# Optimization experiments

Measured on AMD Instinct MI355X. Metric: run time of the kernel, lower is better.

The kernel has to match this reference:

```python
import jax, jax.numpy as jnp
import numpy as np

B, L, D = 4, 2048, 1024
H, DH = 16, 64
W = 128            # window_len
CS, R = 32, 1      # chunk_size, chunk_rank
CACHE = 2048
NCC = CACHE // CS * R   # compressed cache vectors (64)
NCB = L // CS * R       # compressed block vectors (64)
NC = NCC + NCB          # total compressed vectors (128)
NQ = L // CS            # query chunks (64)
T = L // W              # query tiles (16)
NEG = jnp.float32(-1e30)


def _ln(x, g, b, eps=1e-5):
    m = x.mean(-1, keepdims=True)
    v = ((x - m) ** 2).mean(-1, keepdims=True)
    return (x - m) * jax.lax.rsqrt(v + eps) * g + b


def _scores(x, Wd, bd):
    # dconv_1 + per-chunk softmax over chunk_size positions
    b = x.shape[0]; nc = x.shape[1] // CS
    s = (x @ Wd + bd).reshape(b, nc, CS, H, R)
    s = jnp.transpose(s, (0, 3, 1, 4, 2))          # b,H,nc,R,CS
    return jax.nn.softmax(s.astype(jnp.float32), axis=-1).astype(x.dtype)


def _compress(x, sc):
    b = x.shape[0]; nc = x.shape[1] // CS
    xv = jnp.transpose(x.reshape(b, nc, CS, H, DH), (0, 3, 1, 2, 4))  # b,H,nc,CS,DH
    return (sc @ xv).reshape(b, H, nc * R, DH)


def _heads(x):
    b, l, _ = x.shape
    return jnp.transpose(x.reshape(b, l, H, DH), (0, 2, 1, 3))


def _rel_shift(x):
    # Transformer-XL style relative shift, chunk variant (zeros enter from padding)
    b = x.shape[0]; nc = x.shape[-1]
    x5 = jnp.transpose(x.reshape(b, H, NQ, CS, nc), (0, 1, 3, 2, 4))  # b,H,CS,NQ,nc
    xp = jnp.pad(x5, ((0, 0), (0, 0), (0, 0), (0, 0), (0, R))).reshape(b, H, CS, NQ * (nc + R))
    idx = NQ * R + jnp.arange(NQ)[:, None] * nc + jnp.arange(nc)[None, :]
    out = jnp.take(xp, idx.reshape(-1), axis=-1).reshape(b, H, CS, NQ, nc)
    return jnp.transpose(out, (0, 1, 3, 2, 4)).reshape(b, H, L, nc)


def _forward(h, h_cache, key_pe, pos_win, Wq, Wk, Wv, Wo, Wd, bd, Wr, br, Wrc, brc,
             r_r_bias, r_w_bias, g_dproj, b_dproj, g_win, b_win, mask):
    b = h.shape[0]
    q = _heads(h @ Wq) / np.float32(np.sqrt(DH))       # b,H,L,DH (pre-scaled)

    # --- compressed cache keys/values ---
    hcc = _compress(h_cache, _scores(h_cache, Wd, bd))           # b,H,NCC,DH
    hcm = jnp.transpose(hcc, (0, 2, 1, 3)).reshape(b, -1, D)
    k_cache = _heads(_ln(hcm @ Wk, g_dproj, b_dproj))
    v_cache = _heads(_ln(hcm @ Wv, g_dproj, b_dproj))

    # --- sliding window keys/values (last W of cache + current block) ---
    k_bp = h @ Wk
    v_bp = h @ Wv
    hw = h_cache[:, -W:]
    k_win = _ln(jnp.concatenate([hw @ Wk, k_bp], 1), g_win, b_win)   # b, W+L, D
    v_win = _ln(jnp.concatenate([hw @ Wv, v_bp], 1), g_win, b_win)

    # --- compressed current-block keys/values ---
    sc = _scores(h, Wd, bd)
    k_bpc = _heads(_ln(jnp.transpose(_compress(k_bp, sc), (0, 2, 1, 3)).reshape(b, -1, D), g_dproj, b_dproj))
    v_bpc = _heads(_ln(jnp.transpose(_compress(v_bp, sc), (0, 2, 1, 3)).reshape(b, -1, D), g_dproj, b_dproj))
    k_comp = jnp.concatenate([k_cache, k_bpc], 2)     # b,H,NC,DH
    v_comp = jnp.concatenate([v_cache, v_bpc], 2)

    # --- windowed attention (tiled, as_strided equivalent via gather) ---
    ti = jnp.arange(T)[:, None] * W + jnp.arange(2 * W)[None, :]     # (T, 2W)
    k_t = jnp.transpose(k_win[:, ti].reshape(b, T, 2 * W, H, DH), (0, 3, 1, 2, 4))  # b,H,T,2W,DH
    v_t = jnp.transpose(v_win[:, ti].reshape(b, T, 2 * W, H, DH), (0, 3, 1, 2, 4))
    q_t = q.reshape(b, H, T, W, DH)
    aw = jnp.einsum('bhtqd,bhtkd->bhtqk', q_t + r_w_bias, k_t)       # b,H,T,W,2W
    # diagonal extraction: row q keeps cols q+1 .. q+W (the W causal window keys)
    dcol = jnp.arange(W)[:, None] + 1 + jnp.arange(W)[None, :]       # (W, W)
    aw = jnp.take_along_axis(aw, dcol[None, None, None], axis=-1).reshape(b, H, L, W)
    pos_t = (pos_win @ Wr + br).reshape(W, H, DH)
    aw = aw + jnp.einsum('bhld,whd->bhlw', q + r_r_bias, pos_t)

    # --- compressed (chunk) attention ---
    ac = jnp.einsum('bhld,bhcd->bhlc', q, k_comp)
    pos_c = (key_pe @ Wrc + brc).reshape(NC, H, DH)
    ac = ac + _rel_shift(jnp.einsum('bhld,chd->bhlc', q, pos_c))
    ac = jnp.where(mask, NEG, ac.reshape(b, H, NQ, CS, NC)).reshape(b, H, L, NC)

    # --- joint softmax over [compressed | window] ---
    full = jax.nn.softmax(jnp.concatenate([ac, aw], -1).astype(jnp.float32), -1).astype(h.dtype)
    ac, aw = full[..., :NC], full[..., NC:]

    # --- put_tiles: scatter window probs back to tiled 2W layout (inverse of diag extract) ---
    awt = aw.reshape(b, H, T, W, W)
    awp = jnp.pad(awt, ((0, 0), (0, 0), (0, 0), (0, 0), (1, W)))     # last dim 1+2W, zeros outside band
    col = jnp.clip(jnp.arange(2 * W)[None, :] - jnp.arange(W)[:, None], 0, 2 * W)
    aw_t = jnp.take_along_axis(awp, col[None, None, None], axis=-1)  # b,H,T,W,2W

    out = jnp.einsum('bhlc,bhcd->bhld', ac, v_comp) + \
          jnp.einsum('bhtqk,bhtkd->bhtqd', aw_t, v_t).reshape(b, H, L, DH)
    out = jnp.transpose(out, (0, 2, 1, 3)).reshape(b, L, D)
    return out @ Wo


def setup_inputs() -> dict:
    key = jax.random.key(0)
    ks = jax.random.split(key, 16)
    p = lambda i, shape: jax.random.normal(ks[i], shape, jnp.float32) * 0.02
    inp = dict(
        h=jax.random.normal(ks[0], (B, L, D), jnp.float32),
        h_cache=jax.random.normal(ks[1], (B, CACHE, D), jnp.float32),
        key_pe=jax.random.normal(ks[2], (NC, D), jnp.float32),
        pos_embed_window=jax.random.normal(ks[3], (W, D), jnp.float32),
        Wq=p(4, (D, D)), Wk=p(5, (D, D)), Wv=p(6, (D, D)), Wo=p(7, (D, D)),
        Wd=p(8, (D, H * R)), bd=jnp.zeros((H * R,), jnp.float32),
        Wr=p(9, (D, D)), br=jnp.zeros((D,), jnp.float32),
        Wrc=p(10, (D, D)), brc=jnp.zeros((D,), jnp.float32),
        r_r_bias=p(11, (1, H, 1, DH)), r_w_bias=p(12, (1, H, 1, 1, DH)),
        g_dproj=jnp.ones((D,), jnp.float32), b_dproj=jnp.zeros((D,), jnp.float32),
        g_win=jnp.ones((D,), jnp.float32), b_win=jnp.zeros((D,), jnp.float32),
    )
    # causal mask over compressed vectors: bp chunk c visible to query chunk j only if c < j
    jq = jnp.arange(NQ)[:, None]
    cc = jnp.arange(NCB // R)[None, :]
    mbp = jnp.repeat(cc >= jq, R, axis=1)                         # (NQ, NCB)
    mask = jnp.concatenate([jnp.zeros((NQ, NCC), bool), mbp], axis=1)
    inp['chunked_attn_mask'] = mask[None, None, :, None, :]       # (1,1,NQ,1,NC)
    return inp


def reference(h, h_cache, key_pe, pos_embed_window, Wq, Wk, Wv, Wo, Wd, bd, Wr, br,
              Wrc, brc, r_r_bias, r_w_bias, g_dproj, b_dproj, g_win, b_win,
              chunked_attn_mask):
    return _forward(h, h_cache, key_pe, pos_embed_window, Wq, Wk, Wv, Wo, Wd, bd,
                    Wr, br, Wrc, brc, r_r_bias, r_w_bias, g_dproj, b_dproj,
                    g_win, b_win, chunked_attn_mask)
```

## Files before the change

kernel.cpp:

```cpp
#include <hip/hip_runtime.h>


typedef unsigned short u16;
typedef __attribute__((ext_vector_type(8))) short short8;
typedef __attribute__((ext_vector_type(4))) float f32x4;

#define NEGINF -1e30f

__device__ __forceinline__ float bf2f(u16 u) {
    union { unsigned int i; float f; } v; v.i = ((unsigned int)u) << 16; return v.f;
}
__device__ __forceinline__ u16 f2bf(float f) {
    union { float fl; unsigned int i; } v; v.fl = f;
    unsigned int x = v.i;
    return (u16)((x + 0x7fffu + ((x >> 16) & 1u)) >> 16);
}
__device__ __forceinline__ short8 ldg8(const u16* p) { return *(const short8*)p; }

__device__ __forceinline__ void async16(const u16* g, u16* l) {
    __builtin_amdgcn_global_load_lds(
        (const __attribute__((address_space(1))) unsigned int*)g,
        (__attribute__((address_space(3))) unsigned int*)l, 16, 0, 0);
}

__global__ __launch_bounds__(256) void cast_fuse(
    const float* __restrict__ h, const float* __restrict__ hc,
    const float* __restrict__ pos_w, const float* __restrict__ key_pe,
    const float* __restrict__ Wd,
    u16* __restrict__ hB, u16* __restrict__ hcwB,
    u16* __restrict__ pwB, u16* __restrict__ kpeB, u16* __restrict__ WdB,
    const float* __restrict__ W0, const float* __restrict__ W1,
    const float* __restrict__ W2, const float* __restrict__ W3,
    const float* __restrict__ W4, const float* __restrict__ W5,
    u16* __restrict__ D0, u16* __restrict__ D1, u16* __restrict__ D2,
    u16* __restrict__ D3, u16* __restrict__ D4, u16* __restrict__ D5)
{
    const int bx = blockIdx.x, tid = threadIdx.x;
    __shared__ float t[32][33];

    if (bx < 8192) {
        int i = bx * 256 + tid;
        float4 v = ((const float4*)h)[i];
        u16* o = hB + (long)i * 4;
        o[0] = f2bf(v.x); o[1] = f2bf(v.y); o[2] = f2bf(v.z); o[3] = f2bf(v.w);
    } else if (bx < 8704) {
        int i = (bx - 8192) * 256 + tid;
        int flat = i * 4;
        int b = flat >> 17, r = (flat >> 10) & 127, c = flat & 1023;
        float4 v = *(const float4*)(hc + ((long)b * 2048 + 1920 + r) * 1024 + c);
        u16* o = hcwB + (long)flat;
        o[0] = f2bf(v.x); o[1] = f2bf(v.y); o[2] = f2bf(v.z); o[3] = f2bf(v.w);
    } else if (bx < 8832) {
        int i = (bx - 8704) * 256 + tid;
        float4 v = ((const float4*)pos_w)[i];
        u16* o = pwB + (long)i * 4;
        o[0] = f2bf(v.x); o[1] = f2bf(v.y); o[2] = f2bf(v.z); o[3] = f2bf(v.w);
    } else if (bx < 8960) {
        int i = (bx - 8832) * 256 + tid;
        float4 v = ((const float4*)key_pe)[i];
        u16* o = kpeB + (long)i * 4;
        o[0] = f2bf(v.x); o[1] = f2bf(v.y); o[2] = f2bf(v.z); o[3] = f2bf(v.w);
    } else if (bx < 9024) {
        int e = (bx - 8960) * 256 + tid;
        if (e < 16384) WdB[(e & 15) * 1024 + (e >> 4)] = f2bf(Wd[e]);
    } else {
        const int t6 = bx - 9024;
        const int z = t6 >> 10;
        const int rem = t6 & 1023;
        const int bxx = rem & 31, byy = rem >> 5;
        const float* W = (z == 0) ? W0 : (z == 1) ? W1 : (z == 2) ? W2
                       : (z == 3) ? W3 : (z == 4) ? W4 : W5;
        u16* WT = (z == 0) ? D0 : (z == 1) ? D1 : (z == 2) ? D2
                : (z == 3) ? D3 : (z == 4) ? D4 : D5;
        const int tx = tid & 31, ty = tid >> 5;
        #pragma unroll
        for (int p = 0; p < 4; ++p) {
            int k = byy * 32 + ty + p * 8;
            t[ty + p * 8][tx] = W[(long)k * 1024 + bxx * 32 + tx];
        }
        __syncthreads();
        #pragma unroll
        for (int p = 0; p < 4; ++p) {
            int n = ty + p * 8;
            WT[((long)(bxx * 32 + n)) * 1024 + byy * 32 + tx] = f2bf(t[tx][n]);
        }
    }
}

__global__ __launch_bounds__(512) void gemm_qkv_big(
    const u16* __restrict__ A, const u16* __restrict__ Bt,
    u16* __restrict__ q_ws, u16* __restrict__ kbp, u16* __restrict__ vbp)
{
    const int tid = threadIdx.x;
    const int bm = blockIdx.x, bn = blockIdx.y;
    const int K = 1024, NT = 32;

    __shared__ __align__(16) u16 smem[65536 / 2];
    u16* const As = smem;
    u16* const Bs = smem + 16384;

    const int lane = tid & 63, wv = tid >> 6;
    const int l15 = lane & 15, quad = lane >> 4;
    const int wm = (wv >> 2) * 128, wn = (wv & 3) * 64;

    f32x4 acc[8][4];
    #pragma unroll
    for (int i = 0; i < 8; ++i)
        #pragma unroll
        for (int j = 0; j < 4; ++j) acc[i][j] = (f32x4){0.f, 0.f, 0.f, 0.f};

    const int r_in = lane >> 2;
    const int col8 = (((lane & 3) ^ ((lane >> 3) & 3)) * 8);
    const bool isA = (wv < 4);
    const int crow0 = (isA ? wv : wv - 4) * 64;
    const u16* gb = isA ? (A + (long)(bm * 256 + crow0 + r_in) * K)
                        : (Bt + (long)(bn * 256 + crow0 + r_in) * K);
    const u16* s0 = gb + col8;
    const u16* s1 = s0 + (long)16 * K;
    const u16* s2 = s0 + (long)32 * K;
    const u16* s3 = s0 + (long)48 * K;
    u16* const lb = (isA ? As : Bs) + crow0 * 32;

    auto stage = [&](int buf) {
        u16* d = lb + buf * 8192;
        async16(s0, d);
        async16(s1, d + 512);
        async16(s2, d + 1024);
        async16(s3, d + 1536);
        s0 += 32; s1 += 32; s2 += 32; s3 += 32;
    };

    const int ssl = (quad ^ ((l15 >> 1) & 3)) * 8;

    stage(0);
    for (int t = 0; t < NT; ++t) {
        __builtin_amdgcn_s_barrier();
        if (t + 1 < NT) {
            stage((t + 1) & 1);
            asm volatile("s_waitcnt vmcnt(4) lgkmcnt(0)\ns_barrier" ::: "memory");
        } else {
            asm volatile("s_waitcnt vmcnt(0) lgkmcnt(0)\ns_barrier" ::: "memory");
        }
        const u16* as = As + (t & 1) * 8192;
        const u16* bs = Bs + (t & 1) * 8192;
        short8 af[8], bfr[4];
        #pragma unroll
        for (int i = 0; i < 8; ++i)
            af[i] = *(const short8*)&as[(wm + i * 16 + l15) * 32 + ssl];
        #pragma unroll
        for (int j = 0; j < 4; ++j)
            bfr[j] = *(const short8*)&bs[(wn + j * 16 + l15) * 32 + ssl];
        #pragma unroll
// ... 62 lines not shown
        async16(a_src  + k0, &As[cur * 4096 + lofs0]);                          \
        async16(a_src2 + k0, &As[cur * 4096 + lofs1]);                          \
        async16(b_src  + k0, &Bs[cur * 4096 + lofs0]);                          \
        async16(b_src2 + k0, &Bs[cur * 4096 + lofs1]);                          \
    };                                                                          \
    stage(0, 0); stage(1, 1);                                                   \
    const int ssl = (quad ^ ((l15 >> 1) & 3)) * 8;                              \
    int cur = 0;                                                                \
    for (int t = 0; t < NT; ++t) {                                              \
        if (t == NT - 1)                                                        \
            asm volatile("s_waitcnt vmcnt(0) lgkmcnt(0)\ns_barrier" ::: "memory"); \
        else                                                                    \
            asm volatile("s_waitcnt vmcnt(4) lgkmcnt(0)\ns_barrier" ::: "memory"); \
        int nxt = cur + 2; if (nxt >= 3) nxt -= 3;                              \
        if (t + 2 < NT) stage(t + 2, nxt);                                      \
        const u16* as = &As[cur * 4096];                                        \
        const u16* bs = &Bs[cur * 4096];                                        \
        short8 af[4], bfr[4];                                                   \
        _Pragma("unroll")                                                       \
        for (int i = 0; i < 4; ++i)                                             \
            af[i] = *(const short8*)&as[(wm + i * 16 + l15) * 32 + ssl];        \
        _Pragma("unroll")                                                       \
        for (int j = 0; j < 4; ++j)                                             \
            bfr[j] = *(const short8*)&bs[(wn + j * 16 + l15) * 32 + ssl];       \
        _Pragma("unroll")                                                       \
        for (int i = 0; i < 4; ++i)                                             \
            _Pragma("unroll")                                                   \
            for (int j = 0; j < 4; ++j)                                         \
                acc[i][j] = __builtin_amdgcn_mfma_f32_16x16x32_bf16(af[i], bfr[j], acc[i][j], 0, 0, 0); \
        cur = (cur + 1 == 3) ? 0 : cur + 1;                                     \
    }                                                                           \
    EPILOGUE

__global__ __launch_bounds__(256) void gemm_out3(
    const u16* __restrict__ A, const u16* __restrict__ Bt,
    float* __restrict__ Cf)
{
    GEMM_P3_BODY({
        _Pragma("unroll")
        for (int i = 0; i < 4; ++i) {
            _Pragma("unroll")
            for (int j = 0; j < 4; ++j) {
                int col = bn * 128 + wn + j * 16 + l15;
                _Pragma("unroll")
                for (int r = 0; r < 4; ++r) {
                    int row = bm * 128 + wm + i * 16 + quad * 4 + r;
                    Cf[(long)row * 1024 + col] = acc[i][j][r];
                }
            }
        }
    })
}

struct GJob {
    const u16* A; long ab;
    const u16* Bt;
    float* Cf; u16* Cb; long cb;
    const float* bias; float scale;
    int bmN;
};

__device__ __forceinline__ void gemm_core128(
    const GJob& j, int bz, int bm, int bn, int N, int K)
{
    const int tid = threadIdx.x;
    const u16* A = j.A + (long)bz * j.ab;
    const long coff = (long)bz * j.cb;

    __shared__ __align__(16) u16 As[128 * 32];
    __shared__ __align__(16) u16 Bs[128 * 32];

    const int lane = tid & 63, wv = tid >> 6;
    const int l15 = lane & 15, quad = lane >> 4;
    const int wm = (wv & 1) * 64, wn = (wv >> 1) * 64;

    f32x4 acc[4][4];
    #pragma unroll
    for (int i = 0; i < 4; ++i)
        #pragma unroll
        for (int jx = 0; jx < 4; ++jx) acc[i][jx] = (f32x4){0.f, 0.f, 0.f, 0.f};

    const int srow = wv * 32 + (lane >> 2);
    const int scol = (lane & 3) * 8;
    const u16* a_src  = A    + (long)(bm * 128 + srow) * K + scol;
    const u16* a_src2 = a_src + (long)16 * K;
    const u16* b_src  = j.Bt + (long)(bn * 128 + srow) * K + scol;
    const u16* b_src2 = b_src + (long)16 * K;
    u16* lA0 = &As[(wv * 32) * 32];
    u16* lA1 = &As[(wv * 32 + 16) * 32];
    u16* lB0 = &Bs[(wv * 32) * 32];
    u16* lB1 = &Bs[(wv * 32 + 16) * 32];

    for (int k0 = 0; k0 < K; k0 += 32) {
        async16(a_src, lA0); async16(a_src2, lA1);
        async16(b_src, lB0); async16(b_src2, lB1);
        a_src += 32; a_src2 += 32; b_src += 32; b_src2 += 32;
        __syncthreads();
        short8 af[4], bfr[4];
        #pragma unroll
        for (int i = 0; i < 4; ++i)
            af[i] = *(const short8*)&As[(wm + i * 16 + l15) * 32 + quad * 8];
        #pragma unroll
        for (int jx = 0; jx < 4; ++jx)
            bfr[jx] = *(const short8*)&Bs[(wn + jx * 16 + l15) * 32 + quad * 8];
        #pragma unroll
        for (int i = 0; i < 4; ++i)
            #pragma unroll
            for (int jx = 0; jx < 4; ++jx)
                acc[i][jx] = __builtin_amdgcn_mfma_f32_16x16x32_bf16(af[i], bfr[jx], acc[i][jx], 0, 0, 0);
        __syncthreads();
    }

    #pragma unroll
    for (int i = 0; i < 4; ++i) {
        #pragma unroll
        for (int jx = 0; jx < 4; ++jx) {
            int col = bn * 128 + wn + jx * 16 + l15;
            float bsv = j.bias ? j.bias[col] : 0.f;
            #pragma unroll
            for (int r = 0; r < 4; ++r) {
                int row = bm * 128 + wm + i * 16 + quad * 4 + r;
                float v = acc[i][jx][r] * j.scale + bsv;
                long idx = coff + (long)row * N + col;
                if (j.Cf) j.Cf[idx] = v;
                if (j.Cb) j.Cb[idx] = f2bf(v);
            }
        }
    }
}

__global__ __launch_bounds__(256) void gemm_multi6(
    GJob j0, GJob j1, GJob j2, GJob j3, GJob j4, GJob j5,
    int n0, int n1, int n2, int n3, int n4, int N, int K)
{
    const int z = blockIdx.z;
    GJob j; int bz;
    if (z < n0)                          { j = j0; bz = z; }
    else if (z < n0 + n1)                { j = j1; bz = z - n0; }
    else if (z < n0 + n1 + n2)           { j = j2; bz = z - n0 - n1; }
    else if (z < n0 + n1 + n2 + n3)      { j = j3; bz = z - n0 - n1 - n2; }
    else if (z < n0 + n1 + n2 + n3 + n4) { j = j4; bz = z - n0 - n1 - n2 - n3; }
    else                                 { j = j5; bz = z - n0 - n1 - n2 - n3 - n4; }
    if ((int)blockIdx.x >= j.bmN) return;
    gemm_core128(j, bz, blockIdx.x, blockIdx.y, N, K);
}

__global__ __launch_bounds__(256) void scores_compress2(
    const float* __restrict__ hc, const u16* __restrict__ hBp,
    const u16* __restrict__ WdB, const float* __restrict__ bd,
    u16* __restrict__ hcm, float* __restrict__ sc_blk)
{
    const int c = blockIdx.x, b = blockIdx.y;
    const bool zc = (blockIdx.z == 0);
    const int tid = threadIdx.x;
    const int lane = tid & 63, wv = tid >> 6;
    const int l15 = lane & 15, quad = lane >> 4;

    __shared__ __align__(16) u16 srcs[32][1032];
    __shared__ float sred[4][32][16];
    __shared__ float s_sm[32][16];
    __shared__ float smx[4][16];
    __shared__ float ssum[4][16];

    if (zc) {
        const float* sb = hc + (long)b * 2048 * 1024 + (long)c * 32 * 1024;
        for (int e = tid; e < 8192; e += 256) {
            int flat = e * 4;
            int row = flat >> 10, col = flat & 1023;
            float4 v = *(const float4*)(sb + (long)row * 1024 + col);
            u16* dp = &srcs[row][col];
            dp[0] = f2bf(v.x); dp[1] = f2bf(v.y); dp[2] = f2bf(v.z); dp[3] = f2bf(v.w);
        }
    } else {
        const u16* sb = hBp + (long)b * 2048 * 1024 + (long)c * 32 * 1024;
        for (int e = tid; e < 4096; e += 256) {
            int flat = e * 8;
            int row = flat >> 10, col = flat & 1023;
            *(short8*)&srcs[row][col] = ldg8(sb + (long)row * 1024 + col);
        }
    }
    __syncthreads();

    {
        f32x4 acc0 = {0.f,0.f,0.f,0.f}, acc1 = {0.f,0.f,0.f,0.f};
        const int kq = wv * 256;
        #pragma unroll
        for (int kc = 0; kc < 8; ++kc) {
            int off = kq + kc * 32 + quad * 8;
            short8 bf_ = ldg8(WdB + (long)l15 * 1024 + off);
            short8 a0 = *(const short8*)&srcs[l15][off];
            short8 a1 = *(const short8*)&srcs[16 + l15][off];
            acc0 = __builtin_amdgcn_mfma_f32_16x16x32_bf16(a0, bf_, acc0, 0, 0, 0);
            acc1 = __builtin_amdgcn_mfma_f32_16x16x32_bf16(a1, bf_, acc1, 0, 0, 0);
        }
        #pragma unroll
        for (int r = 0; r < 4; ++r) {
            sred[wv][quad * 4 + r][l15]      = acc0[r];
            sred[wv][16 + quad * 4 + r][l15] = acc1[r];
        }
    }
    __syncthreads();
    for (int idx = tid; idx < 512; idx += 256) {
        int i = idx >> 4, hd = idx & 15;
        s_sm[i][hd] = bd[hd] + sred[0][i][hd] + sred[1][i][hd]
                            + sred[2][i][hd] + sred[3][i][hd];
    }
    __syncthreads();

    {
        const int hd = tid & 15, i2 = tid >> 4;
        float a = s_sm[i2][hd], bx = s_sm[i2 + 16][hd];
        float m = fmaxf(a, bx);
        m = fmaxf(m, __shfl_xor(m, 16));
        m = fmaxf(m, __shfl_xor(m, 32));
        if (lane < 16) smx[wv][lane] = m;
        __syncthreads();
        float M = fmaxf(fmaxf(smx[0][hd], smx[1][hd]), fmaxf(smx[2][hd], smx[3][hd]));
        float ea = __expf(a - M), eb = __expf(bx - M);
        float s = ea + eb;
        s += __shfl_xor(s, 16);
        s += __shfl_xor(s, 32);
        if (lane < 16) ssum[wv][lane] = s;
        __syncthreads();
        float S = ssum[0][hd] + ssum[1][hd] + ssum[2][hd] + ssum[3][hd];
        float inv = 1.f / S;
        s_sm[i2][hd]      = ea * inv;
        s_sm[i2 + 16][hd] = eb * inv;
    }
    __syncthreads();

    if (!zc) {
        for (int idx = tid; idx < 512; idx += 256) {
            int hd = idx >> 5, i = idx & 31;
            sc_blk[(long)b * (16*64*32) + ((long)hd * 64 + c) * 32 + i] = s_sm[i][hd];
        }
    } else {
        const int g = tid >> 1, half = tid & 1;
        const int j0 = g * 8;
        const int hd = g >> 3;
        float acc[8] = {0.f,0.f,0.f,0.f,0.f,0.f,0.f,0.f};
        #pragma unroll
        for (int i = 0; i < 16; ++i) {
            const int row = half * 16 + i;
            const float w = s_sm[row][hd];
            short8 sv = *(const short8*)&srcs[row][j0];
            #pragma unroll
            for (int k = 0; k < 8; ++k) acc[k] += w * bf2f((u16)sv[k]);
        }
        #pragma unroll
        for (int k = 0; k < 8; ++k) acc[k] += __shfl_xor(acc[k], 1);
        if (half == 0) {
            u16 o[8];
            #pragma unroll
            for (int k = 0; k < 8; ++k) o[k] = f2bf(acc[k]);
            *(uint4*)&hcm[(long)b * (64*1024) + (long)c * 1024 + j0] = *(const uint4*)o;
        }
    }
}

__global__ __launch_bounds__(256) void post_qkv(
    const float* __restrict__ kcw, const float* __restrict__ vcw,
    const u16* __restrict__ kbp, const u16* __restrict__ vbp,
    float2* __restrict__ st_k, float2* __restrict__ st_v,
    const float* __restrict__ sc,
    const float* __restrict__ kc, const float* __restrict__ vc,
    const float* __restrict__ g, const float* __restrict__ be,
    u16* __restrict__ k_comp, u16* __restrict__ vcT)
{
    const int gr = blockIdx.x;
    const int tid = threadIdx.x;
    const int lane = tid & 63, wv = tid >> 6;

    if (gr < 8704) {
        float sm1 = 0.f, sq1 = 0.f, sm2 = 0.f, sq2 = 0.f;
        long dst;
        if (gr < 512) {
            const int b = gr >> 7, r = gr & 127;
            const float* p1 = kcw + ((long)b * 128 + r) * 1024;
            const float* p2 = vcw + ((long)b * 128 + r) * 1024;
            #pragma unroll
            for (int p = 0; p < 4; ++p) {
                float x = p1[tid + p * 256];
                float y = p2[tid + p * 256];
                sm1 += x; sq1 += x * x;
                sm2 += y; sq2 += y * y;
            }
            dst = (long)b * 2176 + r;
        } else {
            const int g2 = gr - 512;
            const int b = g2 >> 11, r = g2 & 2047;
            const u16* p1 = kbp + ((long)b * 2048 + r) * 1024 + tid * 4;
            const u16* p2 = vbp + ((long)b * 2048 + r) * 1024 + tid * 4;
            uint2 v1 = *(const uint2*)p1;
            uint2 v2 = *(const uint2*)p2;
            const u16* a1 = (const u16*)&v1;
            const u16* a2 = (const u16*)&v2;
            #pragma unroll
            for (int p = 0; p < 4; ++p) {
                float x = bf2f(a1[p]);
                float y = bf2f(a2[p]);
                sm1 += x; sq1 += x * x;
                sm2 += y; sq2 += y * y;
            }
            dst = (long)b * 2176 + 128 + r;
        }

        __shared__ float red[4][4];
        for (int off = 32; off; off >>= 1) {
            sm1 += __shfl_xor(sm1, off); sq1 += __shfl_xor(sq1, off);
            sm2 += __shfl_xor(sm2, off); sq2 += __shfl_xor(sq2, off);
        }
        if (lane == 0) { red[0][wv] = sm1; red[1][wv] = sq1; red[2][wv] = sm2; red[3][wv] = sq2; }
// ... 165 lines not shown
    __syncthreads();
    #pragma unroll
    for (int pass = 0; pass < 16; ++pass) {
        int dd = (tid >> 6) + pass * 4;
        int rr = tid & 63;
        int crow = t0 + rr;
        if (crow >= 1)
            vwinT[((long)b * 1024 + d0 + dd) * 2176 + crow - 1] = vt[rr][dd];
    }
}

__global__ __launch_bounds__(256, 4) void attention(
    const u16* __restrict__ qb,
    const u16* __restrict__ kcb,
    const u16* __restrict__ vcT,
    const u16* __restrict__ kwb,
    const u16* __restrict__ vwT,
    const u16* __restrict__ pcb,
    const u16* __restrict__ ptb,
    const float* __restrict__ r_w,
    const float* __restrict__ r_r,
    u16* __restrict__ attn_o)
{
    const int h = blockIdx.x, qc = blockIdx.y, b = blockIdx.z;
    const int l0 = qc * 32;
    const int tid = threadIdx.x;
    const int lane = tid & 63, wv = tid >> 6;
    const int l15 = lane & 15, quad = lane >> 4;

    __shared__ __align__(16) float L[32 * 260];
    __shared__ __align__(16) u16 qa[32][72];
    u16* Lu = (u16*)L;

    {
        const int r = tid >> 3, d0 = (tid & 7) * 8;
        short8 qv = ldg8(qb + ((long)(b * 2048 + l0 + r)) * 1024 + h * 64 + d0);
        *(short8*)&qa[r][d0] = qv;
    }

    short8 s1k[3][2];
    int nw = 0;
    #pragma unroll
    for (int i = 0; i < 3; ++i) {
        const int nt = wv + i * 4;
        if (nt < 10) {
            int t = nt * 16 + l15;
            int row = l0 + 1 + t; if (row > 2175) row = 2175;
            const u16* kp = kwb + ((long)(b * 2176 + row)) * 1024 + h * 64 + quad * 8;
            s1k[i][0] = ldg8(kp);
            s1k[i][1] = ldg8(kp + 32);
            nw = i + 1;
        }
    }
    __syncthreads();

    __builtin_amdgcn_s_setprio(1);
    #pragma unroll
    for (int ti = 0; ti < 2; ++ti) {
        int n0 = (wv * 2 + ti) * 16;
        int ci = n0 + l15;
        f32x4 a0 = {0.f,0.f,0.f,0.f}, a1 = {0.f,0.f,0.f,0.f};
        if (n0 < 64 + qc) {
            int p = 64 + ci - qc; if (p > 127) p = 127;
            #pragma unroll
            for (int kc = 0; kc < 2; ++kc) {
                int k0 = kc * 32;
                short8 bk = ldg8(kcb + ((long)(b * 128 + ci)) * 1024 + h * 64 + k0 + quad * 8);
                short8 bp = ldg8(pcb + (long)p * 1024 + h * 64 + k0 + quad * 8);
                short8 fa0 = *(const short8*)&qa[l15][k0 + quad * 8];
                short8 fa1 = *(const short8*)&qa[16 + l15][k0 + quad * 8];
                a0 = __builtin_amdgcn_mfma_f32_16x16x32_bf16(fa0, bk, a0, 0, 0, 0);
                a0 = __builtin_amdgcn_mfma_f32_16x16x32_bf16(fa0, bp, a0, 0, 0, 0);
                a1 = __builtin_amdgcn_mfma_f32_16x16x32_bf16(fa1, bk, a1, 0, 0, 0);
                a1 = __builtin_amdgcn_mfma_f32_16x16x32_bf16(fa1, bp, a1, 0, 0, 0);
            }
        }
        bool msk = (ci >= 64 + qc);
        #pragma unroll
        for (int r = 0; r < 4; ++r) {
            L[(quad * 4 + r) * 260 + ci]      = msk ? NEGINF : a0[r];
            L[(16 + quad * 4 + r) * 260 + ci] = msk ? NEGINF : a1[r];
        }
    }

    {
        short8 qf[2][2];
        #pragma unroll
        for (int kc = 0; kc < 2; ++kc) {
            const int off = kc * 32 + quad * 8;
            const float* bp_ = r_r + h * 64 + off;
            float4 b0 = *(const float4*)bp_;
            float4 b1 = *(const float4*)(bp_ + 4);
            float bb[8] = {b0.x,b0.y,b0.z,b0.w,b1.x,b1.y,b1.z,b1.w};
            #pragma unroll
            for (int hf = 0; hf < 2; ++hf) {
                short8 qv = *(const short8*)&qa[hf * 16 + l15][off];
                short8 f;
                #pragma unroll
                for (int j = 0; j < 8; ++j) f[j] = (short)f2bf(bf2f((u16)qv[j]) + bb[j]);
                qf[kc][hf] = f;
            }
        }
        #pragma unroll
        for (int ti = 0; ti < 2; ++ti) {
            int w0 = (wv * 2 + ti) * 16;
            int w = w0 + l15;
            f32x4 a0 = {0.f,0.f,0.f,0.f}, a1 = {0.f,0.f,0.f,0.f};
            #pragma unroll
            for (int kc = 0; kc < 2; ++kc) {
                int k0 = kc * 32;
                short8 bp = ldg8(ptb + (long)w * 1024 + h * 64 + k0 + quad * 8);
                a0 = __builtin_amdgcn_mfma_f32_16x16x32_bf16(qf[kc][0], bp, a0, 0, 0, 0);
                a1 = __builtin_amdgcn_mfma_f32_16x16x32_bf16(qf[kc][1], bp, a1, 0, 0, 0);
            }
            #pragma unroll
            for (int r = 0; r < 4; ++r) {
                L[(quad * 4 + r) * 260 + 128 + w]      = a0[r];
                L[(16 + quad * 4 + r) * 260 + 128 + w] = a1[r];
            }
        }
    }

    f32x4 s1a[3], s1b[3];
    {
        short8 qf[2][2];
        #pragma unroll
        for (int kc = 0; kc < 2; ++kc) {
// ... 129 lines not shown
    const float* Wrc     = (const float*)d_in[12];
    const float* brc     = (const float*)d_in[13];
    const float* r_r     = (const float*)d_in[14];
    const float* r_w     = (const float*)d_in[15];
    const float* g_d     = (const float*)d_in[16];
    const float* b_d     = (const float*)d_in[17];
    const float* g_w     = (const float*)d_in[18];
    const float* b_w     = (const float*)d_in[19];

    char* ws = (char*)d_ws;
    size_t off = 0;
    auto alloc = [&](size_t bytes) -> void* {
        void* p = ws + off; off += (bytes + 255) & ~(size_t)255; return p;
    };
    u16* hB     = (u16*)alloc((size_t)8192 * 1024 * 2);
    u16* hcwB   = (u16*)alloc((size_t)4 * 128 * 1024 * 2);
    u16* WqkvT  = (u16*)alloc((size_t)3 * 1024 * 1024 * 2);
    u16* WoT    = (u16*)alloc((size_t)1024 * 1024 * 2);
    u16* WrT    = (u16*)alloc((size_t)1024 * 1024 * 2);
    u16* WrcT   = (u16*)alloc((size_t)1024 * 1024 * 2);
    u16* pwB    = (u16*)alloc((size_t)128 * 1024 * 2);
    u16* kpeB   = (u16*)alloc((size_t)128 * 1024 * 2);
    u16* WdB    = (u16*)alloc((size_t)16 * 1024 * 2);
    u16*   q_ws   = (u16*)alloc((size_t)8192 * 1024 * 2);
    u16*   kbp    = (u16*)alloc((size_t)8192 * 1024 * 2);
    u16*   vbp    = (u16*)alloc((size_t)8192 * 1024 * 2);
    u16*   attn_o = (u16*)alloc((size_t)8192 * 1024 * 2);
    float* kcw    = (float*)alloc((size_t)4 * 128 * 1024 * 4);
    float* vcw    = (float*)alloc((size_t)4 * 128 * 1024 * 4);
    u16*   hcm    = (u16*)alloc((size_t)4 * 64 * 1024 * 2);
    float* kc_raw = (float*)alloc((size_t)4 * 64 * 1024 * 4);
    float* vc_raw = (float*)alloc((size_t)4 * 64 * 1024 * 4);
    float* sc_blk = (float*)alloc((size_t)4 * 16 * 64 * 32 * 4);
    u16*   k_comp = (u16*)alloc((size_t)4 * 128 * 1024 * 2);
    u16*   vcT    = (u16*)alloc((size_t)4 * 1024 * 128 * 2);
    float2* st_kw = (float2*)alloc((size_t)4 * 2176 * 8);
    float2* st_vw = (float2*)alloc((size_t)4 * 2176 * 8);
    u16*   pos_tb = (u16*)alloc((size_t)128 * 1024 * 2);
    u16*   pos_cb = (u16*)alloc((size_t)128 * 1024 * 2);
    u16*   kwin   = (u16*)alloc((size_t)4 * 2176 * 1024 * 2);
    u16*   vwinT  = (u16*)alloc((size_t)4 * 1024 * 2176 * 2 + 256);

    const u16* WkT = WqkvT + (size_t)1024 * 1024;
    const u16* WvT = WqkvT + (size_t)2 * 1024 * 1024;

    const dim3 blk(256);

    cast_fuse<<<dim3(15168), blk, 0, stream>>>(
        h, h_cache, pos_w, key_pe, Wd, hB, hcwB, pwB, kpeB, WdB,
        Wq, Wk, Wv, Wo, Wr, Wrc,
        WqkvT, WqkvT + (size_t)1024*1024, WqkvT + (size_t)2*1024*1024,
        WoT, WrT, WrcT);

    scores_compress2<<<dim3(64,4,2), blk, 0, stream>>>(h_cache, hB, WdB, bd, hcm, sc_blk);

    {
        GJob jk  = { hcwB, (long)128*1024, WkT, kcw, nullptr, (long)128*1024, nullptr, 1.f, 1 };
        GJob jv  = { hcwB, (long)128*1024, WvT, vcw, nullptr, (long)128*1024, nullptr, 1.f, 1 };
        GJob jt  = { pwB,  0, WrT,  nullptr, pos_tb, 0, br,  1.f, 1 };
        GJob jc  = { kpeB, 0, WrcT, nullptr, pos_cb, 0, brc, 1.f, 1 };
        GJob jkc = { hcm, 0, WkT, kc_raw, nullptr, 0, nullptr, 1.f, 2 };
        GJob jvc = { hcm, 0, WvT, vc_raw, nullptr, 0, nullptr, 1.f, 2 };
        gemm_multi6<<<dim3(2,8,12), blk, 0, stream>>>(jk, jv, jt, jc, jkc, jvc,
                                                      4, 4, 1, 1, 1, 1024, 1024);
    }

    gemm_qkv_big<<<dim3(32,12), dim3(512), 0, stream>>>(hB, WqkvT, q_ws, kbp, vbp);

    post_qkv<<<dim3(9216), blk, 0, stream>>>(kcw, vcw, kbp, vbp, st_kw, st_vw,
                                             sc_blk, kc_raw, vc_raw, g_d, b_d,
                                             k_comp, vcT);

    win_apply<<<dim3(34,16,4), blk, 0, stream>>>(kcw, vcw, kbp, vbp, st_kw, st_vw, g_w, b_w, kwin, vwinT);

    attention<<<dim3(16,64,4), blk, 0, stream>>>(q_ws, k_comp, vcT, kwin, vwinT,
                                                 pos_cb, pos_tb, r_w, r_r, attn_o);
    gemm_out3<<<dim3(64,8,1), blk, 0, stream>>>(attn_o, WoT, (float*)d_out);
}
```

Baseline: 423.2 us.

## Fuse score/compress with independent GEMMs and fold compressed K/V GEMMs into QKV launch

The chunk-score/compress kernel and the four independent projection GEMMs (cache K/V, both positional) now share one launch, using different blockIdx.z slices. The two GEMMs that depend on the compressed cache (kc_raw, vc_raw) become an extra column of blocks in the big QKV GEMM launch. This removes one kernel launch and lets independent work overlap. The attention kernel also loads its compressed-key and positional fragments into registers before the barrier, instead of inside the MFMA loop. In exchange, the fused blocks in the QKV launch run a 256-thread GEMM with 512 threads, so the extra waves do duplicate work, and the merged kernel reserves a large LDS buffer for every block.

```diff
diff --git a/kernel.cpp b/kernel.cpp
--- a/kernel.cpp
+++ b/kernel.cpp
@@ -21,6 +21,71 @@
     __builtin_amdgcn_global_load_lds(
         (const __attribute__((address_space(1))) unsigned int*)g,
         (__attribute__((address_space(3))) unsigned int*)l, 16, 0, 0);
+}
+
+__device__ void gemm128p(u16* As, u16* Bs,
+    const u16* __restrict__ A, const u16* __restrict__ Bt,
+    float* Cf, u16* Cb, const float* bias, float scale,
+    int bm, int bn, int N, int K)
+{
+    const int tid = threadIdx.x;
+    const int lane = tid & 63, wv = (tid >> 6) & 3;
+    const int l15 = lane & 15, quad = lane >> 4;
+    const int wm = (wv & 1) * 64, wn = (wv >> 1) * 64;
+
+    f32x4 acc[4][4];
+    #pragma unroll
+    for (int i = 0; i < 4; ++i)
+        #pragma unroll
+        for (int jx = 0; jx < 4; ++jx) acc[i][jx] = (f32x4){0.f, 0.f, 0.f, 0.f};
+
+    const int srow = wv * 32 + (lane >> 2);
+    const int scol = (lane & 3) * 8;
+    const u16* a_src  = A  + (long)(bm * 128 + srow) * K + scol;
+    const u16* a_src2 = a_src + (long)16 * K;
+    const u16* b_src  = Bt + (long)(bn * 128 + srow) * K + scol;
+    const u16* b_src2 = b_src + (long)16 * K;
+    u16* lA0 = &As[(wv * 32) * 32];
+    u16* lA1 = &As[(wv * 32 + 16) * 32];
+    u16* lB0 = &Bs[(wv * 32) * 32];
+    u16* lB1 = &Bs[(wv * 32 + 16) * 32];
+
+    for (int k0 = 0; k0 < K; k0 += 32) {
+        async16(a_src, lA0); async16(a_src2, lA1);
+        async16(b_src, lB0); async16(b_src2, lB1);
+        a_src += 32; a_src2 += 32; b_src += 32; b_src2 += 32;
+        __syncthreads();
+        short8 af[4], bfr[4];
+        #pragma unroll
+        for (int i = 0; i < 4; ++i)
+            af[i] = *(const short8*)&As[(wm + i * 16 + l15) * 32 + quad * 8];
+        #pragma unroll
+        for (int jx = 0; jx < 4; ++jx)
+            bfr[jx] = *(const short8*)&Bs[(wn + jx * 16 + l15) * 32 + quad * 8];
+        #pragma unroll
+        for (int i = 0; i < 4; ++i)
+            #pragma unroll
+            for (int jx = 0; jx < 4; ++jx)
+                acc[i][jx] = __builtin_amdgcn_mfma_f32_16x16x32_bf16(af[i], bfr[jx], acc[i][jx], 0, 0, 0);
+        __syncthreads();
+    }
+
+    #pragma unroll
+    for (int i = 0; i < 4; ++i) {
+        #pragma unroll
+        for (int jx = 0; jx < 4; ++jx) {
+            int col = bn * 128 + wn + jx * 16 + l15;
+            float bsv = bias ? bias[col] : 0.f;
+            #pragma unroll
+            for (int r = 0; r < 4; ++r) {
+                int row = bm * 128 + wm + i * 16 + quad * 4 + r;
+                float v = acc[i][jx][r] * scale + bsv;
+                long idx = (long)row * N + col;
+                if (Cf) Cf[idx] = v;
+                if (Cb) Cb[idx] = f2bf(v);
+            }
+        }
+    }
 }
 
 __global__ __launch_bounds__(256) void cast_fuse(
@@ -87,9 +152,154 @@
     }
 }
 
+__global__ __launch_bounds__(256) void scores_multi(
+    const float* __restrict__ hc, const u16* __restrict__ hBp,
+    const u16* __restrict__ WdB, const float* __restrict__ bd,
+    u16* __restrict__ hcm, float* __restrict__ sc_blk,
+    const u16* __restrict__ hcwB, const u16* __restrict__ WkT,
+    const u16* __restrict__ WvT,
+    float* __restrict__ kcw, float* __restrict__ vcw,
+    const u16* __restrict__ pwB, const u16* __restrict__ WrT,
+    u16* __restrict__ pos_tb, const float* __restrict__ br,
+    const u16* __restrict__ kpeB, const u16* __restrict__ WrcT,
+    u16* __restrict__ pos_cb, const float* __restrict__ brc)
+{
+    __shared__ __align__(16) char sm[76800];
+
+    const int tid = threadIdx.x;
+
+    if (blockIdx.z == 2) {
+        const int bx = blockIdx.x, bn = blockIdx.y;
+        if (bx >= 10) return;
+        u16* As = (u16*)sm;
+        u16* Bs = (u16*)(sm + 8192);
+        if (bx < 4)
+            gemm128p(As, Bs, hcwB + (long)bx * 128 * 1024, WkT,
+                     kcw + (long)bx * 128 * 1024, nullptr, nullptr, 1.f, 0, bn, 1024, 1024);
+        else if (bx < 8)
+            gemm128p(As, Bs, hcwB + (long)(bx - 4) * 128 * 1024, WvT,
+                     vcw + (long)(bx - 4) * 128 * 1024, nullptr, nullptr, 1.f, 0, bn, 1024, 1024);
+        else if (bx == 8)
+            gemm128p(As, Bs, pwB, WrT, nullptr, pos_tb, br, 1.f, 0, bn, 1024, 1024);
+        else
+            gemm128p(As, Bs, kpeB, WrcT, nullptr, pos_cb, brc, 1.f, 0, bn, 1024, 1024);
+        return;
+    }
+
+    const int c = blockIdx.x, b = blockIdx.y;
+    if (b >= 4) return;
+    const bool zc = (blockIdx.z == 0);
+    const int lane = tid & 63, wv = tid >> 6;
+    const int l15 = lane & 15, quad = lane >> 4;
+
+    u16 (*srcs)[1032]      = (u16 (*)[1032])sm;
+    float (*sred)[32][16]  = (float (*)[32][16])(sm + 66048);
+    float (*s_sm)[16]      = (float (*)[16])(sm + 74240);
+    float (*smx)[16]       = (float (*)[16])(sm + 76288);
+    float (*ssum)[16]      = (float (*)[16])(sm + 76544);
+
+    if (zc) {
+        const float* sb = hc + (long)b * 2048 * 1024 + (long)c * 32 * 1024;
+        for (int e = tid; e < 8192; e += 256) {
+            int flat = e * 4;
+            int row = flat >> 10, col = flat & 1023;
+            float4 v = *(const float4*)(sb + (long)row * 1024 + col);
+            u16* dp = &srcs[row][col];
+            dp[0] = f2bf(v.x); dp[1] = f2bf(v.y); dp[2] = f2bf(v.z); dp[3] = f2bf(v.w);
+        }
+    } else {
+        const u16* sb = hBp + (long)b * 2048 * 1024 + (long)c * 32 * 1024;
+        for (int e = tid; e < 4096; e += 256) {
+            int flat = e * 8;
+            int row = flat >> 10, col = flat & 1023;
+            *(short8*)&srcs[row][col] = ldg8(sb + (long)row * 1024 + col);
+        }
+    }
+    __syncthreads();
+
+    {
+        f32x4 acc0 = {0.f,0.f,0.f,0.f}, acc1 = {0.f,0.f,0.f,0.f};
+        const int kq = wv * 256;
+        #pragma unroll
+        for (int kc = 0; kc < 8; ++kc) {
+            int off = kq + kc * 32 + quad * 8;
+            short8 bf_ = ldg8(WdB + (long)l15 * 1024 + off);
+            short8 a0 = *(const short8*)&srcs[l15][off];
+            short8 a1 = *(const short8*)&srcs[16 + l15][off];
+            acc0 = __builtin_amdgcn_mfma_f32_16x16x32_bf16(a0, bf_, acc0, 0, 0, 0);
+            acc1 = __builtin_amdgcn_mfma_f32_16x16x32_bf16(a1, bf_, acc1, 0, 0, 0);
+        }
+        #pragma unroll
+        for (int r = 0; r < 4; ++r) {
+            sred[wv][quad * 4 + r][l15]      = acc0[r];
+            sred[wv][16 + quad * 4 + r][l15] = acc1[r];
+        }
+    }
+    __syncthreads();
+    for (int idx = tid; idx < 512; idx += 256) {
+        int i = idx >> 4, hd = idx & 15;
+        s_sm[i][hd] = bd[hd] + sred[0][i][hd] + sred[1][i][hd]
+                            + sred[2][i][hd] + sred[3][i][hd];
+    }
+    __syncthreads();
+
+    {
+        const int hd = tid & 15, i2 = tid >> 4;
+        float a = s_sm[i2][hd], bx2 = s_sm[i2 + 16][hd];
+        float m = fmaxf(a, bx2);
+        m = fmaxf(m, __shfl_xor(m, 16));
+        m = fmaxf(m, __shfl_xor(m, 32));
+        if (lane < 16) smx[wv][lane] = m;
+        __syncthreads();
+        float M = fmaxf(fmaxf(smx[0][hd], smx[1][hd]), fmaxf(smx[2][hd], smx[3][hd]));
+        float ea = __expf(a - M), eb = __expf(bx2 - M);
+        float s = ea + eb;
+        s += __shfl_xor(s, 16);
+        s += __shfl_xor(s, 32);
+        if (lane < 16) ssum[wv][lane] = s;
+        __syncthreads();
+        float S = ssum[0][hd] + ssum[1][hd] + ssum[2][hd] + ssum[3][hd];
+        float inv = 1.f / S;
+        s_sm[i2][hd]      = ea * inv;
+        s_sm[i2 + 16][hd] = eb * inv;
+    }
+    __syncthreads();
+
+    if (!zc) {
+        for (int idx = tid; idx < 512; idx += 256) {
+            int hd = idx >> 5, i = idx & 31;
+            sc_blk[(long)b * (16*64*32) + ((long)hd * 64 + c) * 32 + i] = s_sm[i][hd];
+        }
+    } else {
+        const int g = tid >> 1, half = tid & 1;
+        const int j0 = g * 8;
+        const int hd = g >> 3;
+        float acc[8] = {0.f,0.f,0.f,0.f,0.f,0.f,0.f,0.f};
+        #pragma unroll
+        for (int i = 0; i < 16; ++i) {
+            const int row = half * 16 + i;
+            const float w = s_sm[row][hd];
+            short8 sv = *(const short8*)&srcs[row][j0];
+            #pragma unroll
+            for (int k = 0; k < 8; ++k) acc[k] += w * bf2f((u16)sv[k]);
+        }
+        #pragma unroll
+        for (int k = 0; k < 8; ++k) acc[k] += __shfl_xor(acc[k], 1);
+        if (half == 0) {
+            u16 o[8];
+            #pragma unroll
+            for (int k = 0; k < 8; ++k) o[k] = f2bf(acc[k]);
+            *(uint4*)&hcm[(long)b * (64*1024) + (long)c * 1024 + j0] = *(const uint4*)o;
+        }
+    }
+}
+
 __global__ __launch_bounds__(512) void gemm_qkv_big(
     const u16* __restrict__ A, const u16* __restrict__ Bt,
-    u16* __restrict__ q_ws, u16* __restrict__ kbp, u16* __restrict__ vbp)
+    u16* __restrict__ q_ws, u16* __restrict__ kbp, u16* __restrict__ vbp,
+    const u16* __restrict__ hcm, const u16* __restrict__ WkT,
+    const u16* __restrict__ WvT,
+    float* __restrict__ kc_raw, float* __restrict__ vc_raw)
 {
     const int tid = threadIdx.x;
     const int bm = blockIdx.x, bn = blockIdx.y;
@@ -98,6 +308,17 @@
     __shared__ __align__(16) u16 smem[65536 / 2];
     u16* const As = smem;
     u16* const Bs = smem + 16384;
+
+    if (bn == 12) {
+        const int job = bm >> 4;
+        const int r = bm & 15;
+        const int bm2 = r >> 3, bn2 = r & 7;
+        if (job == 0)
+            gemm128p(As, As + 4096, hcm, WkT, kc_raw, nullptr, nullptr, 1.f, bm2, bn2, 1024, 1024);
+        else
+            gemm128p(As, As + 4096, hcm, WvT, vc_raw, nullptr, nullptr, 1.f, bm2, bn2, 1024, 1024);
+        return;
+    }
 
     const int lane = tid & 63, wv = tid >> 6;
     const int l15 = lane & 15, quad = lane >> 4;
@@ -266,212 +487,6 @@
     })
 }
 
-struct GJob {
-    const u16* A; long ab;
-    const u16* Bt;
-    float* Cf; u16* Cb; long cb;
-    const float* bias; float scale;
-    int bmN;
-};
-
-__device__ __forceinline__ void gemm_core128(
-    const GJob& j, int bz, int bm, int bn, int N, int K)
-{
-    const int tid = threadIdx.x;
-    const u16* A = j.A + (long)bz * j.ab;
-    const long coff = (long)bz * j.cb;
-
-    __shared__ __align__(16) u16 As[128 * 32];
-    __shared__ __align__(16) u16 Bs[128 * 32];
-
-    const int lane = tid & 63, wv = tid >> 6;
-    const int l15 = lane & 15, quad = lane >> 4;
-    const int wm = (wv & 1) * 64, wn = (wv >> 1) * 64;
-
-    f32x4 acc[4][4];
-    #pragma unroll
-    for (int i = 0; i < 4; ++i)
-        #pragma unroll
-        for (int jx = 0; jx < 4; ++jx) acc[i][jx] = (f32x4){0.f, 0.f, 0.f, 0.f};
-
-    const int srow = wv * 32 + (lane >> 2);
-    const int scol = (lane & 3) * 8;
-    const u16* a_src  = A    + (long)(bm * 128 + srow) * K + scol;
-    const u16* a_src2 = a_src + (long)16 * K;
-    const u16* b_src  = j.Bt + (long)(bn * 128 + srow) * K + scol;
-    const u16* b_src2 = b_src + (long)16 * K;
-    u16* lA0 = &As[(wv * 32) * 32];
-    u16* lA1 = &As[(wv * 32 + 16) * 32];
-    u16* lB0 = &Bs[(wv * 32) * 32];
-    u16* lB1 = &Bs[(wv * 32 + 16) * 32];
-
-    for (int k0 = 0; k0 < K; k0 += 32) {
-        async16(a_src, lA0); async16(a_src2, lA1);
-        async16(b_src, lB0); async16(b_src2, lB1);
-        a_src += 32; a_src2 += 32; b_src += 32; b_src2 += 32;
-        __syncthreads();
-        short8 af[4], bfr[4];
-        #pragma unroll
-        for (int i = 0; i < 4; ++i)
-            af[i] = *(const short8*)&As[(wm + i * 16 + l15) * 32 + quad * 8];
-        #pragma unroll
-        for (int jx = 0; jx < 4; ++jx)
-            bfr[jx] = *(const short8*)&Bs[(wn + jx * 16 + l15) * 32 + quad * 8];
-        #pragma unroll
-        for (int i = 0; i < 4; ++i)
-            #pragma unroll
-            for (int jx = 0; jx < 4; ++jx)
-                acc[i][jx] = __builtin_amdgcn_mfma_f32_16x16x32_bf16(af[i], bfr[jx], acc[i][jx], 0, 0, 0);
-        __syncthreads();
-    }
-
-    #pragma unroll
-    for (int i = 0; i < 4; ++i) {
-        #pragma unroll
-        for (int jx = 0; jx < 4; ++jx) {
-            int col = bn * 128 + wn + jx * 16 + l15;
-            float bsv = j.bias ? j.bias[col] : 0.f;
-            #pragma unroll
-            for (int r = 0; r < 4; ++r) {
-                int row = bm * 128 + wm + i * 16 + quad * 4 + r;
-                float v = acc[i][jx][r] * j.scale + bsv;
-                long idx = coff + (long)row * N + col;
-                if (j.Cf) j.Cf[idx] = v;
-                if (j.Cb) j.Cb[idx] = f2bf(v);
-            }
-        }
-    }
-}
-
-__global__ __launch_bounds__(256) void gemm_multi6(
-    GJob j0, GJob j1, GJob j2, GJob j3, GJob j4, GJob j5,
-    int n0, int n1, int n2, int n3, int n4, int N, int K)
-{
-    const int z = blockIdx.z;
-    GJob j; int bz;
-    if (z < n0)                          { j = j0; bz = z; }
-    else if (z < n0 + n1)                { j = j1; bz = z - n0; }
-    else if (z < n0 + n1 + n2)           { j = j2; bz = z - n0 - n1; }
-    else if (z < n0 + n1 + n2 + n3)      { j = j3; bz = z - n0 - n1 - n2; }
-    else if (z < n0 + n1 + n2 + n3 + n4) { j = j4; bz = z - n0 - n1 - n2 - n3; }
-    else                                 { j = j5; bz = z - n0 - n1 - n2 - n3 - n4; }
-    if ((int)blockIdx.x >= j.bmN) return;
-    gemm_core128(j, bz, blockIdx.x, blockIdx.y, N, K);
-}
-
-__global__ __launch_bounds__(256) void scores_compress2(
-    const float* __restrict__ hc, const u16* __restrict__ hBp,
-    const u16* __restrict__ WdB, const float* __restrict__ bd,
-    u16* __restrict__ hcm, float* __restrict__ sc_blk)
-{
-    const int c = blockIdx.x, b = blockIdx.y;
-    const bool zc = (blockIdx.z == 0);
-    const int tid = threadIdx.x;
-    const int lane = tid & 63, wv = tid >> 6;
-    const int l15 = lane & 15, quad = lane >> 4;
-
-    __shared__ __align__(16) u16 srcs[32][1032];
-    __shared__ float sred[4][32][16];
-    __shared__ float s_sm[32][16];
-    __shared__ float smx[4][16];
-    __shared__ float ssum[4][16];
-
-    if (zc) {
-        const float* sb = hc + (long)b * 2048 * 1024 + (long)c * 32 * 1024;
-        for (int e = tid; e < 8192; e += 256) {
-            int flat = e * 4;
-            int row = flat >> 10, col = flat & 1023;
-            float4 v = *(const float4*)(sb + (long)row * 1024 + col);
-            u16* dp = &srcs[row][col];
-            dp[0] = f2bf(v.x); dp[1] = f2bf(v.y); dp[2] = f2bf(v.z); dp[3] = f2bf(v.w);
-        }
-    } else {
-        const u16* sb = hBp + (long)b * 2048 * 1024 + (long)c * 32 * 1024;
-        for (int e = tid; e < 4096; e += 256) {
-            int flat = e * 8;
-            int row = flat >> 10, col = flat & 1023;
-            *(short8*)&srcs[row][col] = ldg8(sb + (long)row * 1024 + col);
-        }
-    }
-    __syncthreads();
-
-    {
-        f32x4 acc0 = {0.f,0.f,0.f,0.f}, acc1 = {0.f,0.f,0.f,0.f};
-        const int kq = wv * 256;
-        #pragma unroll
-        for (int kc = 0; kc < 8; ++kc) {
-            int off = kq + kc * 32 + quad * 8;
-            short8 bf_ = ldg8(WdB + (long)l15 * 1024 + off);
-            short8 a0 = *(const short8*)&srcs[l15][off];
-            short8 a1 = *(const short8*)&srcs[16 + l15][off];
-            acc0 = __builtin_amdgcn_mfma_f32_16x16x32_bf16(a0, bf_, acc0, 0, 0, 0);
-            acc1 = __builtin_amdgcn_mfma_f32_16x16x32_bf16(a1, bf_, acc1, 0, 0, 0);
-        }
-        #pragma unroll
-        for (int r = 0; r < 4; ++r) {
-            sred[wv][quad * 4 + r][l15]      = acc0[r];
-            sred[wv][16 + quad * 4 + r][l15] = acc1[r];
-        }
-    }
-    __syncthreads();
-    for (int idx = tid; idx < 512; idx += 256) {
-        int i = idx >> 4, hd = idx & 15;
-        s_sm[i][hd] = bd[hd] + sred[0][i][hd] + sred[1][i][hd]
-                            + sred[2][i][hd] + sred[3][i][hd];
-    }
-    __syncthreads();
-
-    {
-        const int hd = tid & 15, i2 = tid >> 4;
-        float a = s_sm[i2][hd], bx = s_sm[i2 + 16][hd];
-        float m = fmaxf(a, bx);
-        m = fmaxf(m, __shfl_xor(m, 16));
-        m = fmaxf(m, __shfl_xor(m, 32));
-        if (lane < 16) smx[wv][lane] = m;
-        __syncthreads();
-        float M = fmaxf(fmaxf(smx[0][hd], smx[1][hd]), fmaxf(smx[2][hd], smx[3][hd]));
-        float ea = __expf(a - M), eb = __expf(bx - M);
-        float s = ea + eb;
-        s += __shfl_xor(s, 16);
-        s += __shfl_xor(s, 32);
-        if (lane < 16) ssum[wv][lane] = s;
-        __syncthreads();
-        float S = ssum[0][hd] + ssum[1][hd] + ssum[2][hd] + ssum[3][hd];
-        float inv = 1.f / S;
-        s_sm[i2][hd]      = ea * inv;
-        s_sm[i2 + 16][hd] = eb * inv;
-    }
-    __syncthreads();
-
-    if (!zc) {
-        for (int idx = tid; idx < 512; idx += 256) {
-            int hd = idx >> 5, i = idx & 31;
-            sc_blk[(long)b * (16*64*32) + ((long)hd * 64 + c) * 32 + i] = s_sm[i][hd];
-        }
-    } else {
-        const int g = tid >> 1, half = tid & 1;
-        const int j0 = g * 8;
-        const int hd = g >> 3;
-        float acc[8] = {0.f,0.f,0.f,0.f,0.f,0.f,0.f,0.f};
-        #pragma unroll
-        for (int i = 0; i < 16; ++i) {
-            const int row = half * 16 + i;
-            const float w = s_sm[row][hd];
-            short8 sv = *(const short8*)&srcs[row][j0];
-            #pragma unroll
-            for (int k = 0; k < 8; ++k) acc[k] += w * bf2f((u16)sv[k]);
-        }
-        #pragma unroll
-        for (int k = 0; k < 8; ++k) acc[k] += __shfl_xor(acc[k], 1);
-        if (half == 0) {
-            u16 o[8];
-            #pragma unroll
-            for (int k = 0; k < 8; ++k) o[k] = f2bf(acc[k]);
-            *(uint4*)&hcm[(long)b * (64*1024) + (long)c * 1024 + j0] = *(const uint4*)o;
-        }
-    }
-}
-
 __global__ __launch_bounds__(256) void post_qkv(
     const float* __restrict__ kcw, const float* __restrict__ vcw,
     const u16* __restrict__ kbp, const u16* __restrict__ vbp,
@@ -743,6 +758,16 @@
             nw = i + 1;
         }
     }
+    short8 sck[2][2], scp[2][2];
+    #pragma unroll
+    for (int ti = 0; ti < 2; ++ti) {
+        const int ci = (wv * 2 + ti) * 16 + l15;
+        int p = 64 + ci - qc; if (p > 127) p = 127;
+        const u16* kp2 = kcb + ((long)(b * 128 + ci)) * 1024 + h * 64 + quad * 8;
+        const u16* pp2 = pcb + (long)p * 1024 + h * 64 + quad * 8;
+        sck[ti][0] = ldg8(kp2); sck[ti][1] = ldg8(kp2 + 32);
+        scp[ti][0] = ldg8(pp2); scp[ti][1] = ldg8(pp2 + 32);
+    }
     __syncthreads();
 
     __builtin_amdgcn_s_setprio(1);
@@ -752,18 +777,15 @@
         int ci = n0 + l15;
         f32x4 a0 = {0.f,0.f,0.f,0.f}, a1 = {0.f,0.f,0.f,0.f};
         if (n0 < 64 + qc) {
-            int p = 64 + ci - qc; if (p > 127) p = 127;
             #pragma unroll
             for (int kc = 0; kc < 2; ++kc) {
                 int k0 = kc * 32;
-                short8 bk = ldg8(kcb + ((long)(b * 128 + ci)) * 1024 + h * 64 + k0 + quad * 8);
-                short8 bp = ldg8(pcb + (long)p * 1024 + h * 64 + k0 + quad * 8);
                 short8 fa0 = *(const short8*)&qa[l15][k0 + quad * 8];
                 short8 fa1 = *(const short8*)&qa[16 + l15][k0 + quad * 8];
-                a0 = __builtin_amdgcn_mfma_f32_16x16x32_bf16(fa0, bk, a0, 0, 0, 0);
-                a0 = __builtin_amdgcn_mfma_f32_16x16x32_bf16(fa0, bp, a0, 0, 0, 0);
-                a1 = __builtin_amdgcn_mfma_f32_16x16x32_bf16(fa1, bk, a1, 0, 0, 0);
-                a1 = __builtin_amdgcn_mfma_f32_16x16x32_bf16(fa1, bp, a1, 0, 0, 0);
+                a0 = __builtin_amdgcn_mfma_f32_16x16x32_bf16(fa0, sck[ti][kc], a0, 0, 0, 0);
+                a0 = __builtin_amdgcn_mfma_f32_16x16x32_bf16(fa0, scp[ti][kc], a0, 0, 0, 0);
+                a1 = __builtin_amdgcn_mfma_f32_16x16x32_bf16(fa1, sck[ti][kc], a1, 0, 0, 0);
+                a1 = __builtin_amdgcn_mfma_f32_16x16x32_bf16(fa1, scp[ti][kc], a1, 0, 0, 0);
             }
         }
         bool msk = (ci >= 64 + qc);
@@ -999,20 +1021,14 @@
         WqkvT, WqkvT + (size_t)1024*1024, WqkvT + (size_t)2*1024*1024,
         WoT, WrT, WrcT);
 
-    scores_compress2<<<dim3(64,4,2), blk, 0, stream>>>(h_cache, hB, WdB, bd, hcm, sc_blk);
-
-    {
-        GJob jk  = { hcwB, (long)128*1024, WkT, kcw, nullptr, (long)128*1024, nullptr, 1.f, 1 };
-        GJob jv  = { hcwB, (long)128*1024, WvT, vcw, nullptr, (long)128*1024, nullptr, 1.f, 1 };
-        GJob jt  = { pwB,  0, WrT,  nullptr, pos_tb, 0, br,  1.f, 1 };
-        GJob jc  = { kpeB, 0, WrcT, nullptr, pos_cb, 0, brc, 1.f, 1 };
-        GJob jkc = { hcm, 0, WkT, kc_raw, nullptr, 0, nullptr, 1.f, 2 };
-        GJob jvc = { hcm, 0, WvT, vc_raw, nullptr, 0, nullptr, 1.f, 2 };
-        gemm_multi6<<<dim3(2,8,12), blk, 0, stream>>>(jk, jv, jt, jc, jkc, jvc,
-                                                      4, 4, 1, 1, 1, 1024, 1024);
-    }
-
-    gemm_qkv_big<<<dim3(32,12), dim3(512), 0, stream>>>(hB, WqkvT, q_ws, kbp, vbp);
+    scores_multi<<<dim3(64,8,3), blk, 0, stream>>>(
+        h_cache, hB, WdB, bd, hcm, sc_blk,
+        hcwB, WkT, WvT, kcw, vcw,
+        pwB, WrT, pos_tb, br,
+        kpeB, WrcT, pos_cb, brc);
+
+    gemm_qkv_big<<<dim3(32,13), dim3(512), 0, stream>>>(hB, WqkvT, q_ws, kbp, vbp,
+                                                        hcm, WkT, WvT, kc_raw, vc_raw);
 
     post_qkv<<<dim3(9216), blk, 0, stream>>>(kcw, vcw, kbp, vbp, st_kw, st_vw,
                                              sc_blk, kc_raw, vc_raw, g_d, b_d,
```

After: 439.3 us. 1.04x slower.
